# Kernel tuning notes

Hardware: AMD Instinct MI355X
Metric: run time of the kernel (lower is better)

## Reference

```python
import jax, jax.numpy as jnp
import numpy as np

N = 100000      # nodes
E = 1600000     # edges
R = 8           # relation types
D = 128         # in_dim = h_dim = out_dim

def setup_inputs() -> dict:
    key = jax.random.key(0)
    ks = jax.random.split(key, 10)
    feats = jax.random.normal(ks[0], (N, D), dtype=jnp.float32)
    src = jax.random.randint(ks[1], (E,), 0, N, dtype=jnp.int32)
    dst = jax.random.randint(ks[2], (E,), 0, N, dtype=jnp.int32)
    etype = jax.random.randint(ks[3], (E,), 0, R, dtype=jnp.int32)
    s = 0.05  # keep activations well-scaled
    W1 = jax.random.normal(ks[4], (R, D, D), dtype=jnp.float32) * s
    loop_w1 = jax.random.normal(ks[5], (D, D), dtype=jnp.float32) * s
    b1 = jnp.zeros((D,), dtype=jnp.float32)
    W2 = jax.random.normal(ks[6], (R, D, D), dtype=jnp.float32) * s
    loop_w2 = jax.random.normal(ks[7], (D, D), dtype=jnp.float32) * s
    b2 = jnp.zeros((D,), dtype=jnp.float32)
    return {"feats": feats, "W1": W1, "loop_w1": loop_w1, "b1": b1,
            "W2": W2, "loop_w2": loop_w2, "b2": b2,
            "src": src, "dst": dst, "etype": etype}

def _rel_conv(h, W, loop_w, b, src, dst, etype, relu):
    # Per-relation transform of all node features: [R, N, out]
    # (cheaper than gathering a per-edge [E, in, out] weight tensor)
    h_rel = jnp.einsum('ni,rio->rno', h, W)
    # Per-edge message = W_{etype(e)} @ h[src(e)] : [E, out]
    msg = h_rel[etype, src]
    # Sum-aggregate messages at destination nodes
    agg = jax.ops.segment_sum(msg, dst, num_segments=h.shape[0])
    out = agg + h @ loop_w + b  # self-loop + bias
    return jax.nn.relu(out) if relu else out

def reference(feats, W1, loop_w1, b1, W2, loop_w2, b2, src, dst, etype):
    # eval-mode forward: dropout is identity
    h = _rel_conv(feats, W1, loop_w1, b1, src, dst, etype, relu=True)
    h = _rel_conv(h, W2, loop_w2, b2, src, dst, etype, relu=False)
    return h
```

## Files before the change

### kernel.cpp

```cpp
#include <hip/hip_runtime.h>
#include <hip/hip_bf16.h>


#define D 128
#define KTOT 1152
#define KACC 1024
#define BK 32
#define BSH 9
#define BSZ 512

typedef __attribute__((ext_vector_type(8))) __bf16 bf16x8;
typedef __attribute__((ext_vector_type(8))) unsigned short us8;
typedef __attribute__((ext_vector_type(4))) unsigned short us4;
typedef __attribute__((ext_vector_type(4))) float f32x4;

__device__ __forceinline__ unsigned short f2bf(float f) {
    union { float f; unsigned u; } v; v.f = f;
    unsigned r = v.u + 0x7FFF + ((v.u >> 16) & 1);
    return (unsigned short)(r >> 16);
}
__device__ __forceinline__ float bf2f(unsigned short u) {
    return __uint_as_float((unsigned)u << 16);
}

__device__ __forceinline__ int lds_off(int row, int c) {
    return row * 32 + ((c ^ ((row >> 1) & 3)) << 3);
}


__global__ __launch_bounds__(256) void histA_kernel(const int* __restrict__ dst,
                                                    int* __restrict__ bcnt, int E, int nbuck) {
    __shared__ int c[1024];
    int t = threadIdx.x;
    for (int i = t; i < nbuck; i += 256) c[i] = 0;
    __syncthreads();
    int stride = gridDim.x * 256;
    for (int e = blockIdx.x * 256 + t; e < E; e += stride)
        atomicAdd(&c[dst[e] >> BSH], 1);
    __syncthreads();
    for (int i = t; i < nbuck; i += 256)
        if (c[i]) atomicAdd(&bcnt[i], c[i]);
}

__global__ __launch_bounds__(1024) void scanA_kernel(const int* __restrict__ bcnt,
                                                     int* __restrict__ boffs,
                                                     int* __restrict__ bhead, int nbuck) {
    int t = threadIdx.x;
    int v = (t < nbuck) ? bcnt[t] : 0;
    int lane = t & 63, w = t >> 6;
    int inc = v;
    #pragma unroll
    for (int off = 1; off < 64; off <<= 1) {
        int n = __shfl_up(inc, off, 64);
        if (lane >= off) inc += n;
    }
    __shared__ int ws[16];
    if (lane == 63) ws[w] = inc;
    __syncthreads();
    int wbase = 0;
    for (int i = 0; i < w; ++i) wbase += ws[i];
    int ex = wbase + inc - v;
    if (t < nbuck) { boffs[t] = ex; bhead[t] = ex; }
    if (t == nbuck - 1) boffs[nbuck] = ex + v;
}

__global__ __launch_bounds__(256) void scatterA_kernel(const int* __restrict__ src,
                                                       const int* __restrict__ dst,
                                                       const int* __restrict__ et,
                                                       int* __restrict__ bhead,
                                                       int* __restrict__ sortedA, int E, int nbuck) {
    const int TILE = 4096;
    __shared__ int skey[TILE];
    __shared__ unsigned short sbkt[TILE];
    __shared__ int cnt[1024];
    __shared__ int lpos[1024];
    __shared__ int gdelta[1024];
    __shared__ int ws[4];
    const int t = threadIdx.x;
    const int e0 = blockIdx.x * TILE;
    int dreg[16];

    for (int i = t; i < nbuck; i += 256) cnt[i] = 0;
    __syncthreads();
    #pragma unroll
    for (int j = 0; j < 16; ++j) {
        int e = e0 + j * 256 + t;
        int d = -1;
        if (e < E) { d = dst[e]; atomicAdd(&cnt[d >> BSH], 1); }
        dreg[j] = d;
    }
    __syncthreads();
    int b0 = t * 4;
    int c0 = 0, c1 = 0, c2 = 0, c3 = 0;
    if (b0     < nbuck) c0 = cnt[b0];
    if (b0 + 1 < nbuck) c1 = cnt[b0 + 1];
    if (b0 + 2 < nbuck) c2 = cnt[b0 + 2];
    if (b0 + 3 < nbuck) c3 = cnt[b0 + 3];
    int s = c0 + c1 + c2 + c3;
    int lane = t & 63, w = t >> 6;
    int inc = s;
    #pragma unroll
    for (int off = 1; off < 64; off <<= 1) {
        int n = __shfl_up(inc, off, 64);
        if (lane >= off) inc += n;
    }
    if (lane == 63) ws[w] = inc;
    __syncthreads();
    int wbase = 0;
    for (int i = 0; i < w; ++i) wbase += ws[i];
    int ex = wbase + inc - s;
    int l0 = ex, l1 = ex + c0, l2 = ex + c0 + c1, l3 = ex + c0 + c1 + c2;
    if (b0     < nbuck) { lpos[b0]     = l0; if (c0) gdelta[b0]     = atomicAdd(&bhead[b0],     c0) - l0; }
    if (b0 + 1 < nbuck) { lpos[b0 + 1] = l1; if (c1) gdelta[b0 + 1] = atomicAdd(&bhead[b0 + 1], c1) - l1; }
    if (b0 + 2 < nbuck) { lpos[b0 + 2] = l2; if (c2) gdelta[b0 + 2] = atomicAdd(&bhead[b0 + 2], c2) - l2; }
    if (b0 + 3 < nbuck) { lpos[b0 + 3] = l3; if (c3) gdelta[b0 + 3] = atomicAdd(&bhead[b0 + 3], c3) - l3; }
    __syncthreads();
    #pragma unroll
    for (int j = 0; j < 16; ++j) {
        int e = e0 + j * 256 + t;
        if (e < E) {
            int d = dreg[j];
            int b = d >> BSH;
            int key = ((d & (BSZ - 1)) << 20) | (et[e] << 17) | src[e];
            int p = atomicAdd(&lpos[b], 1);
            skey[p] = key;
            sbkt[p] = (unsigned short)b;
        }
    }
    __syncthreads();
    int ntile = min(TILE, E - e0);
    for (int i = t; i < ntile; i += 256)
        sortedA[gdelta[sbkt[i]] + i] = skey[i];
}


__global__ __launch_bounds__(256) void passB_kernel(const int* __restrict__ sortedA,
                                                    const int* __restrict__ boffs,
                                                    int* __restrict__ sorted,
                                                    int* __restrict__ offs2,
                                                    int N8, int E, int nbuck) {
    __shared__ int cnt[4096];
    __shared__ int cur[4096];
    __shared__ int ws[4];
    const int b = blockIdx.x;
    const int t = threadIdx.x;
    const int gb0 = boffs[b], gb1 = boffs[b + 1];
    #pragma unroll
    for (int i = 0; i < 16; ++i) cnt[i * 256 + t] = 0;
    __syncthreads();
    for (int e = gb0 + t; e < gb1; e += 256) {
        int k = sortedA[e];
        atomicAdd(&cnt[(k >> 17) & 4095], 1);
    }
    __syncthreads();
    const int base = t * 16;
    int s = 0;
    #pragma unroll
    for (int i = 0; i < 16; ++i) s += cnt[base + i];
    int lane = t & 63, w = t >> 6;
    int inc = s;
    #pragma unroll
    for (int off = 1; off < 64; off <<= 1) {
        int n = __shfl_up(inc, off, 64);
        if (lane >= off) inc += n;
    }
    if (lane == 63) ws[w] = inc;
    __syncthreads();
    int wbase = 0;
    for (int i = 0; i < w; ++i) wbase += ws[i];
    int run = gb0 + wbase + inc - s;
    int g0 = (b << 12) + base;
    #pragma unroll
    for (int i = 0; i < 16; ++i) {
        int cv = cnt[base + i];
        cur[base + i] = run;
        if (g0 + i <= N8) offs2[g0 + i] = run;
        run += cv;
    }
    __syncthreads();
    for (int e = gb0 + t; e < gb1; e += 256) {
        int k = sortedA[e];
        int p = atomicAdd(&cur[(k >> 17) & 4095], 1);
        sorted[p] = k;
    }
}


__global__ void cast_kernel(const float* __restrict__ W1, const float* __restrict__ lw1,
                            const float* __restrict__ W2, const float* __restrict__ lw2,
                            const float* __restrict__ feats,
                            unsigned short* __restrict__ Bt1, unsigned short* __restrict__ Bt2,
                            unsigned short* __restrict__ hb0, int n4) {
    const int per = KTOT * D;
    int idx = blockIdx.x * blockDim.x + threadIdx.x;
    if (idx < 2 * per) {
        int layer = idx / per;
        int rem = idx - layer * per;
        int k = rem >> 7;
        int o = rem & 127;
        const float* W  = layer ? W2 : W1;
        const float* lw = layer ? lw2 : lw1;
        float val = (k < 1024) ? W[k * D + o] : lw[(k - 1024) * D + o];
        unsigned short* Bt = layer ? Bt2 : Bt1;
        Bt[o * KTOT + k] = f2bf(val);
    } else {
        int i = idx - 2 * per;
        if (i < n4) {
            float4 v = *(const float4*)(feats + (size_t)i * 4);
            us4 o; o.x = f2bf(v.x); o.y = f2bf(v.y); o.z = f2bf(v.z); o.w = f2bf(v.w);
            *(us4*)(hb0 + (size_t)i * 4) = o;
        }
    }
}


__global__ __launch_bounds__(256) void aggregate_kernel(const unsigned short* __restrict__ hb,
                                                        const int* __restrict__ offs2,
                                                        const int* __restrict__ sorted,
                                                        unsigned short* __restrict__ A,
                                                        int v0, int vend) {
    const int t = threadIdx.x;
    const int u = t >> 4;
    const int c = (t & 15) * 8;
    const int v = v0 + blockIdx.x * 16 + u;
    if (v >= vend) return;

    const int* o2 = offs2 + (size_t)v * 8;
    unsigned short* Ab = A + (size_t)(v - v0) * KACC + c;
    int e0 = o2[0];
    #pragma unroll
    for (int r = 0; r < 8; ++r) {
        int e1 = o2[r + 1];
        float a[8];
        #pragma unroll
        for (int j = 0; j < 8; ++j) a[j] = 0.f;
        #pragma unroll 2
        for (int e = e0; e < e1; ++e) {
            int p = sorted[e];
            int s = p & 131071;
            us8 hv = *(const us8*)(hb + (size_t)s * D + c);
            #pragma unroll
            for (int j = 0; j < 8; ++j) a[j] += bf2f(hv[j]);
        }
        us8 o;
        #pragma unroll
        for (int j = 0; j < 8; ++j) o[j] = f2bf(a[j]);
        *(us8*)(Ab + r * 128) = o;
        e0 = e1;
    }
}


__global__ __launch_bounds__(256) void gemm_kernel(const unsigned short* __restrict__ A,
                                                   const unsigned short* __restrict__ hbA,
                                                   const unsigned short* __restrict__ Bt,
                                                   const float* __restrict__ bias,
                                                   float* __restrict__ outf,
                                                   unsigned short* __restrict__ outb,
                                                   int v0, int vend, int relu_bf) {
    __shared__ unsigned short Alds[64 * 32];
    __shared__ unsigned short Blds[128 * 32];
    const int t = threadIdx.x;
    const int lane = t & 63;
    const int w = t >> 6;
    const int quad = lane >> 4;
    const int c16 = lane & 15;
    const int blockRow0 = v0 + blockIdx.x * 64;

    const int srow = t >> 2;
    const int schunk = t & 3;

    f32x4 acc[8];
    #pragma unroll
    for (int j = 0; j < 8; ++j) acc[j] = f32x4{0.f, 0.f, 0.f, 0.f};

    const int aRow = blockRow0 + srow;
    const bool aval = aRow < vend;
    const us8 zz = {0, 0, 0, 0, 0, 0, 0, 0};
    const unsigned short* Arow = A + (size_t)(aRow - v0) * KACC + schunk * 8;
    const unsigned short* Hrow = hbA + (size_t)aRow * D + schunk * 8;
    const unsigned short* Brow0 = Bt + (size_t)srow * KTOT + schunk * 8;
    const unsigned short* Brow1 = Bt + (size_t)(srow + 64) * KTOT + schunk * 8;

    us8 av = zz;
    if (aval) av = *(const us8*)(Arow);
    us8 bv0 = *(const us8*)(Brow0);
    us8 bv1 = *(const us8*)(Brow1);

    for (int k0 = 0; k0 < KTOT; k0 += BK) {
        us8 na = zz, nb0 = zz, nb1 = zz;
        const int kn = k0 + BK;
        if (kn < KTOT) {
            if (aval) {
                if (kn < KACC) na = *(const us8*)(Arow + kn);
                else           na = *(const us8*)(Hrow + (kn - KACC));
            }
            nb0 = *(const us8*)(Brow0 + kn);
            nb1 = *(const us8*)(Brow1 + kn);
        }
        __syncthreads();
        *(us8*)(Alds + lds_off(srow, schunk)) = av;
        *(us8*)(Blds + lds_off(srow,      schunk)) = bv0;
        *(us8*)(Blds + lds_off(srow + 64, schunk)) = bv1;
        __syncthreads();

        bf16x8 af = *(const bf16x8*)(Alds + lds_off(w * 16 + c16, quad));
        #pragma unroll
        for (int ct = 0; ct < 8; ++ct) {
            bf16x8 bfr = *(const bf16x8*)(Blds + lds_off(ct * 16 + c16, quad));
            acc[ct] = __builtin_amdgcn_mfma_f32_16x16x32_bf16(af, bfr, acc[ct], 0, 0, 0);
        }
        av = na; bv0 = nb0; bv1 = nb1;
    }

    int row = blockRow0 + w * 16 + quad * 4;
    #pragma unroll
    for (int ct = 0; ct < 8; ++ct) {
        int col = ct * 16 + c16;
        float bcol = bias[col];
        #pragma unroll
        for (int i = 0; i < 4; ++i) {
            int r = row + i;
            if (r < vend) {
                float vv = acc[ct][i] + bcol;
                if (relu_bf) {
                    vv = fmaxf(vv, 0.f);
                    outb[(size_t)r * D + col] = f2bf(vv);
                } else {
                    outf[(size_t)r * D + col] = vv;
                }
            }
        }
    }
}


extern "C" void kernel_launch(void* const* d_in, const int* in_sizes, int n_in,
                              void* d_out, int out_size, void* d_ws, size_t ws_size,
                              hipStream_t stream) {
    const float* feats = (const float*)d_in[0];
    const float* W1    = (const float*)d_in[1];
    const float* lw1   = (const float*)d_in[2];
    const float* b1    = (const float*)d_in[3];
    const float* W2    = (const float*)d_in[4];
    const float* lw2   = (const float*)d_in[5];
    const float* b2    = (const float*)d_in[6];
    const int*   src   = (const int*)d_in[7];
    const int*   dst   = (const int*)d_in[8];
    const int*   etype = (const int*)d_in[9];
    const int N = in_sizes[0] / D;
    const int E = in_sizes[7];
    float* out = (float*)d_out;

    const int ch = (N + 1) / 2;
    const int nbuck = (N + BSZ - 1) >> BSH;

    size_t woff = 0;
    auto take = [&](size_t bytes) -> void* {
        void* p = (char*)d_ws + woff;
        woff += (bytes + 255) & ~(size_t)255;
        return p;
    };
    int* bcnt           = (int*)take((size_t)1024 * 4);
    int* boffs          = (int*)take((size_t)1025 * 4);
    int* bhead          = (int*)take((size_t)1024 * 4);
    int* offs2          = (int*)take((size_t)(N * 8 + 1) * 4);
    int* sortedA        = (int*)take((size_t)E * 4);
    int* sorted         = (int*)take((size_t)E * 4);
    unsigned short* Bt1 = (unsigned short*)take((size_t)KTOT * D * 2);
    unsigned short* Bt2 = (unsigned short*)take((size_t)KTOT * D * 2);
    unsigned short* hb0 = (unsigned short*)take((size_t)N * D * 2);
    unsigned short* hb1 = (unsigned short*)take((size_t)N * D * 2);
    unsigned short* ACC = (unsigned short*)take((size_t)ch * KACC * 2);

    (void)hipMemsetAsync(bcnt, 0, (size_t)nbuck * 4, stream);

    histA_kernel<<<1024, 256, 0, stream>>>(dst, bcnt, E, nbuck);
    scanA_kernel<<<1, 1024, 0, stream>>>(bcnt, boffs, bhead, nbuck);
    scatterA_kernel<<<(E + 4095) / 4096, 256, 0, stream>>>(src, dst, etype, bhead, sortedA, E, nbuck);
    passB_kernel<<<nbuck, 256, 0, stream>>>(sortedA, boffs, sorted, offs2, N * 8, E, nbuck);

    int n4 = N * D / 4;
    int cb = (2 * KTOT * D + n4 + 255) / 256;
    cast_kernel<<<cb, 256, 0, stream>>>(W1, lw1, W2, lw2, feats, Bt1, Bt2, hb0, n4);

    for (int layer = 0; layer < 2; ++layer) {
        const unsigned short* hin = layer ? hb1 : hb0;
        const unsigned short* Bt  = layer ? Bt2 : Bt1;
        const float* bias         = layer ? b2  : b1;
        for (int c0 = 0; c0 < N; c0 += ch) {
            int c1 = (c0 + ch < N) ? (c0 + ch) : N;
            int len = c1 - c0;
            int ab = (len + 15) / 16;
            int gb = (len + 63) / 64;
            aggregate_kernel<<<ab, 256, 0, stream>>>(hin, offs2, sorted, ACC, c0, c1);
            gemm_kernel<<<gb, 256, 0, stream>>>(ACC, hin, Bt, bias, out, hb1, c0, c1, 1 - layer);
        }
    }
}
```

Before: 575.4 us.

## Fuse per-relation aggregation into GEMM kernel with double-buffered LDS tiles

Replaces the separate aggregate and GEMM kernels, which passed through a chunked bf16 ACC buffer in global memory, with one fused kernel per layer. Each 64-row block gathers the per-relation neighbour sums for one relation slice into LDS, double-buffered so the next gather overlaps the current MFMA pass. B fragments are now read straight from global memory (L2) instead of being staged in LDS. This removes the ACC write/read traffic and extra launches, but mixes latency-bound gathers with MFMA work in one block and drops LDS reuse of the weights.

Result: slower. 1.018 ms (+76.9%).

```diff
diff --git a/kernel.cpp b/kernel.cpp
--- a/kernel.cpp
+++ b/kernel.cpp
@@ -4,8 +4,6 @@
 
 #define D 128
 #define KTOT 1152
-#define KACC 1024
-#define BK 32
 #define BSH 9
 #define BSZ 512
 
@@ -23,8 +21,8 @@
     return __uint_as_float((unsigned)u << 16);
 }
 
-__device__ __forceinline__ int lds_off(int row, int c) {
-    return row * 32 + ((c ^ ((row >> 1) & 3)) << 3);
+__device__ __forceinline__ int aoff(int row, int chunk) {
+    return row * 128 + ((chunk ^ (row & 15)) << 3);
 }
 
 
@@ -214,106 +212,78 @@
 }
 
 
-__global__ __launch_bounds__(256) void aggregate_kernel(const unsigned short* __restrict__ hb,
-                                                        const int* __restrict__ offs2,
-                                                        const int* __restrict__ sorted,
-                                                        unsigned short* __restrict__ A,
-                                                        int v0, int vend) {
-    const int t = threadIdx.x;
-    const int u = t >> 4;
-    const int c = (t & 15) * 8;
-    const int v = v0 + blockIdx.x * 16 + u;
-    if (v >= vend) return;
-
-    const int* o2 = offs2 + (size_t)v * 8;
-    unsigned short* Ab = A + (size_t)(v - v0) * KACC + c;
-    int e0 = o2[0];
-    #pragma unroll
-    for (int r = 0; r < 8; ++r) {
-        int e1 = o2[r + 1];
-        float a[8];
-        #pragma unroll
-        for (int j = 0; j < 8; ++j) a[j] = 0.f;
-        #pragma unroll 2
-        for (int e = e0; e < e1; ++e) {
-            int p = sorted[e];
-            int s = p & 131071;
-            us8 hv = *(const us8*)(hb + (size_t)s * D + c);
-            #pragma unroll
-            for (int j = 0; j < 8; ++j) a[j] += bf2f(hv[j]);
-        }
-        us8 o;
-        #pragma unroll
-        for (int j = 0; j < 8; ++j) o[j] = f2bf(a[j]);
-        *(us8*)(Ab + r * 128) = o;
-        e0 = e1;
-    }
-}
-
-
-__global__ __launch_bounds__(256) void gemm_kernel(const unsigned short* __restrict__ A,
-                                                   const unsigned short* __restrict__ hbA,
-                                                   const unsigned short* __restrict__ Bt,
-                                                   const float* __restrict__ bias,
-                                                   float* __restrict__ outf,
-                                                   unsigned short* __restrict__ outb,
-                                                   int v0, int vend, int relu_bf) {
-    __shared__ unsigned short Alds[64 * 32];
-    __shared__ unsigned short Blds[128 * 32];
+__global__ __launch_bounds__(256) void fused_kernel(const unsigned short* __restrict__ hb,
+                                                    const int* __restrict__ offs2,
+                                                    const int* __restrict__ sorted,
+                                                    const unsigned short* __restrict__ Bt,
+                                                    const float* __restrict__ bias,
+                                                    float* __restrict__ outf,
+                                                    unsigned short* __restrict__ outb,
+                                                    int N, int relu_bf) {
+    __shared__ unsigned short Asl[2][64 * 128];
     const int t = threadIdx.x;
     const int lane = t & 63;
     const int w = t >> 6;
     const int quad = lane >> 4;
     const int c16 = lane & 15;
-    const int blockRow0 = v0 + blockIdx.x * 64;
-
-    const int srow = t >> 2;
-    const int schunk = t & 3;
+    const int unit = t >> 4;
+    const int l16 = t & 15;
+    const int v0 = blockIdx.x * 64;
 
     f32x4 acc[8];
     #pragma unroll
     for (int j = 0; j < 8; ++j) acc[j] = f32x4{0.f, 0.f, 0.f, 0.f};
 
-    const int aRow = blockRow0 + srow;
-    const bool aval = aRow < vend;
-    const us8 zz = {0, 0, 0, 0, 0, 0, 0, 0};
-    const unsigned short* Arow = A + (size_t)(aRow - v0) * KACC + schunk * 8;
-    const unsigned short* Hrow = hbA + (size_t)aRow * D + schunk * 8;
-    const unsigned short* Brow0 = Bt + (size_t)srow * KTOT + schunk * 8;
-    const unsigned short* Brow1 = Bt + (size_t)(srow + 64) * KTOT + schunk * 8;
-
-    us8 av = zz;
-    if (aval) av = *(const us8*)(Arow);
-    us8 bv0 = *(const us8*)(Brow0);
-    us8 bv1 = *(const us8*)(Brow1);
-
-    for (int k0 = 0; k0 < KTOT; k0 += BK) {
-        us8 na = zz, nb0 = zz, nb1 = zz;
-        const int kn = k0 + BK;
-        if (kn < KTOT) {
-            if (aval) {
-                if (kn < KACC) na = *(const us8*)(Arow + kn);
-                else           na = *(const us8*)(Hrow + (kn - KACC));
+    auto gather = [&](int rr, int buf) {
+        #pragma unroll
+        for (int i = 0; i < 4; ++i) {
+            int row = unit * 4 + i;
+            int v = v0 + row;
+            us8 ov = {0, 0, 0, 0, 0, 0, 0, 0};
+            if (rr == 8) {
+                if (v < N) ov = *(const us8*)(hb + (size_t)v * D + l16 * 8);
+            } else {
+                float a[8];
+                #pragma unroll
+                for (int j = 0; j < 8; ++j) a[j] = 0.f;
+                if (v < N) {
+                    int e0 = offs2[v * 8 + rr], e1 = offs2[v * 8 + rr + 1];
+                    #pragma unroll 4
+                    for (int e = e0; e < e1; ++e) {
+                        int p = sorted[e];
+                        int s = p & 131071;
+                        us8 hv = *(const us8*)(hb + (size_t)s * D + l16 * 8);
+                        #pragma unroll
+                        for (int j = 0; j < 8; ++j) a[j] += bf2f(hv[j]);
+                    }
+                }
+                #pragma unroll
+                for (int j = 0; j < 8; ++j) ov[j] = f2bf(a[j]);
             }
-            nb0 = *(const us8*)(Brow0 + kn);
-            nb1 = *(const us8*)(Brow1 + kn);
+            *(us8*)(&Asl[buf][0] + aoff(row, l16)) = ov;
+        }
+    };
+
+    gather(0, 0);
+    __syncthreads();
+
+    for (int r = 0; r < 9; ++r) {
+        if (r < 8) gather(r + 1, (r + 1) & 1);
+        const unsigned short* As = &Asl[r & 1][0];
+        #pragma unroll
+        for (int ks = 0; ks < 4; ++ks) {
+            bf16x8 af = *(const bf16x8*)(As + aoff(w * 16 + c16, ks * 4 + quad));
+            #pragma unroll
+            for (int ct = 0; ct < 8; ++ct) {
+                bf16x8 bfr = *(const bf16x8*)(Bt + (size_t)(ct * 16 + c16) * KTOT
+                                              + r * 128 + ks * 32 + quad * 8);
+                acc[ct] = __builtin_amdgcn_mfma_f32_16x16x32_bf16(af, bfr, acc[ct], 0, 0, 0);
+            }
         }
         __syncthreads();
-        *(us8*)(Alds + lds_off(srow, schunk)) = av;
-        *(us8*)(Blds + lds_off(srow,      schunk)) = bv0;
-        *(us8*)(Blds + lds_off(srow + 64, schunk)) = bv1;
-        __syncthreads();
-
-        bf16x8 af = *(const bf16x8*)(Alds + lds_off(w * 16 + c16, quad));
-        #pragma unroll
-        for (int ct = 0; ct < 8; ++ct) {
-            bf16x8 bfr = *(const bf16x8*)(Blds + lds_off(ct * 16 + c16, quad));
-            acc[ct] = __builtin_amdgcn_mfma_f32_16x16x32_bf16(af, bfr, acc[ct], 0, 0, 0);
-        }
-        av = na; bv0 = nb0; bv1 = nb1;
-    }
-
-    int row = blockRow0 + w * 16 + quad * 4;
+    }
+
+    int row = v0 + w * 16 + quad * 4;
     #pragma unroll
     for (int ct = 0; ct < 8; ++ct) {
         int col = ct * 16 + c16;
@@ -321,7 +291,7 @@
         #pragma unroll
         for (int i = 0; i < 4; ++i) {
             int r = row + i;
-            if (r < vend) {
+            if (r < N) {
                 float vv = acc[ct][i] + bcol;
                 if (relu_bf) {
                     vv = fmaxf(vv, 0.f);
@@ -352,7 +322,6 @@
     const int E = in_sizes[7];
     float* out = (float*)d_out;
 
-    const int ch = (N + 1) / 2;
     const int nbuck = (N + BSZ - 1) >> BSH;
 
     size_t woff = 0;
@@ -371,7 +340,6 @@
     unsigned short* Bt2 = (unsigned short*)take((size_t)KTOT * D * 2);
     unsigned short* hb0 = (unsigned short*)take((size_t)N * D * 2);
     unsigned short* hb1 = (unsigned short*)take((size_t)N * D * 2);
-    unsigned short* ACC = (unsigned short*)take((size_t)ch * KACC * 2);
 
     (void)hipMemsetAsync(bcnt, 0, (size_t)nbuck * 4, stream);
 
@@ -384,17 +352,7 @@
     int cb = (2 * KTOT * D + n4 + 255) / 256;
     cast_kernel<<<cb, 256, 0, stream>>>(W1, lw1, W2, lw2, feats, Bt1, Bt2, hb0, n4);
 
-    for (int layer = 0; layer < 2; ++layer) {
-        const unsigned short* hin = layer ? hb1 : hb0;
-        const unsigned short* Bt  = layer ? Bt2 : Bt1;
-        const float* bias         = layer ? b2  : b1;
-        for (int c0 = 0; c0 < N; c0 += ch) {
-            int c1 = (c0 + ch < N) ? (c0 + ch) : N;
-            int len = c1 - c0;
-            int ab = (len + 15) / 16;
-            int gb = (len + 63) / 64;
-            aggregate_kernel<<<ab, 256, 0, stream>>>(hin, offs2, sorted, ACC, c0, c1);
-            gemm_kernel<<<gb, 256, 0, stream>>>(ACC, hin, Bt, bias, out, hb1, c0, c1, 1 - layer);
-        }
-    }
-}
+    int fb = (N + 63) / 64;
+    fused_kernel<<<fb, 256, 0, stream>>>(hb0, offs2, sorted, Bt1, b1, nullptr, hb1, N, 1);
+    fused_kernel<<<fb, 256, 0, stream>>>(hb1, offs2, sorted, Bt2, b2, out, nullptr, N, 0);
+}
```
